# Performance work log

Measured on AMD Instinct MI355X. Metric: run time of the kernel, lower is better.

The kernel has to match this reference:

```python
import jax, jax.numpy as jnp
import numpy as np

N = 100_000   # nodes
E = 1_600_000 # edges (COO, directed as given)
D = 128       # input feature dim
H = 128       # hidden dim
L = 3         # layers


def setup_inputs() -> dict:
    key = jax.random.key(0)
    ks = jax.random.split(key, 2 + 2 * L)
    x = jax.random.normal(ks[0], (N, D), dtype=jnp.float32)
    edge_index = jax.random.randint(ks[1], (2, E), 0, N, dtype=jnp.int32)
    inp = {"x": x, "edge_index": edge_index}
    dims = [(D, H), (H, H), (H, H)]
    for i, (fi, fo) in enumerate(dims):
        scale = 1.0 / np.sqrt(fi)
        inp[f"W{i}"] = jax.random.uniform(ks[2 + 2 * i], (fi, fo), jnp.float32, -scale, scale)
        inp[f"b{i}"] = jax.random.uniform(ks[3 + 2 * i], (fo,), jnp.float32, -scale, scale)
    return inp


def reference(x, edge_index, W0, b0, W1, b1, W2, b2):
    n = x.shape[0]
    src, dst = edge_index[0], edge_index[1]
    # GCNConv default: add self-loops, symmetric D^{-1/2}(A+I)D^{-1/2} normalization
    loop = jnp.arange(n, dtype=edge_index.dtype)
    src = jnp.concatenate([src, loop])
    dst = jnp.concatenate([dst, loop])
    ones = jnp.ones(src.shape[0], dtype=x.dtype)
    deg = jax.ops.segment_sum(ones, dst, num_segments=n)          # [N]
    dinv = jnp.where(deg > 0, jax.lax.rsqrt(deg), 0.0)            # deg^{-1/2}, inf->0
    norm = dinv[src] * dinv[dst]                                  # [E+N]

    def gcn_conv(h, W, b):
        h = h @ W                                  # linear transform first (PyG order)
        msg = h[src] * norm[:, None]               # gather + scale, [E+N, H]
        return jax.ops.segment_sum(msg, dst, num_segments=n) + b

    for W, b in ((W0, b0), (W1, b1), (W2, b2)):
        x = jax.nn.relu(gcn_conv(x, W, b))
    return x
```

## Files before the change

### kernel.cpp

```cpp
#include <hip/hip_runtime.h>
#include <hip/hip_bf16.h>

#define TPB 256

typedef short s8v __attribute__((ext_vector_type(8)));
typedef float f4v __attribute__((ext_vector_type(4)));
typedef _Float16 h8v __attribute__((ext_vector_type(8)));

#define PB 128
#define BSHIFT 10
#define BSPAN 1024
#define PCHUNK 4096

__device__ __forceinline__ unsigned short bf16_rne(float v) {
    unsigned int u = __float_as_uint(v);
    u += 0x7fffu + ((u >> 16) & 1u);
    return (unsigned short)(u >> 16);
}
__device__ __forceinline__ void split_bf16(float v, unsigned short& hi, unsigned short& lo) {
    hi = bf16_rne(v);
    float hf = __uint_as_float((unsigned int)hi << 16);
    lo = bf16_rne(v - hf);
}


__global__ __launch_bounds__(256) void bhist_kernel(const int* __restrict__ dst, int E,
                                                    int* __restrict__ bsize) {
    __shared__ int h[PB];
    int t = threadIdx.x;
    if (t < PB) h[t] = 0;
    __syncthreads();
    for (int e = blockIdx.x * 256 + t; e < E; e += gridDim.x * 256)
        atomicAdd(&h[dst[e] >> BSHIFT], 1);
    __syncthreads();
    if (t < PB && h[t] > 0) atomicAdd(&bsize[t], h[t]);
}

__global__ void bscan_kernel(const int* __restrict__ bsize, int* __restrict__ bbase,
                             int* __restrict__ bcursor, int* __restrict__ row, int n, int E) {
    __shared__ int wtot[2];
    int t = threadIdx.x;
    int sz = bsize[t];
    int lane = t & 63, wid = t >> 6;
    int v = sz;
    for (int off = 1; off < 64; off <<= 1) {
        int u = __shfl_up(v, off);
        if (lane >= off) v += u;
    }
    if (lane == 63) wtot[wid] = v;
    __syncthreads();
    if (wid == 1) v += wtot[0];
    bbase[t + 1] = v;
    bcursor[t] = v - sz;
    if (t == 0) { bbase[0] = 0; row[n] = E; }
}

__global__ __launch_bounds__(256) void partition_kernel(const int* __restrict__ src,
                                                        const int* __restrict__ dst, int E,
                                                        int* __restrict__ bcursor,
                                                        int2* __restrict__ part) {
    __shared__ int h[PB];
    __shared__ int gofs[PB];
    int t = threadIdx.x;
    long base = (long)blockIdx.x * PCHUNK;
    int cnt = (int)min((long)PCHUNK, (long)E - base);

    if (t < PB) h[t] = 0;
    __syncthreads();
    for (int j = t; j < cnt; j += 256)
        atomicAdd(&h[dst[base + j] >> BSHIFT], 1);
    __syncthreads();
    if (t < PB) gofs[t] = (h[t] > 0) ? atomicAdd(&bcursor[t], h[t]) : 0;
    __syncthreads();
    if (t < PB) h[t] = 0;
    __syncthreads();
    for (int j = t; j < cnt; j += 256) {
        int s = src[base + j], d = dst[base + j];
        int b = d >> BSHIFT;
        int idx = atomicAdd(&h[b], 1);
        part[(long)gofs[b] + idx] = make_int2(s, d);
    }
}

__global__ __launch_bounds__(1024) void csr_kernel(const int2* __restrict__ part,
                                                   const int* __restrict__ bbase,
                                                   int* __restrict__ row, float* __restrict__ dinv,
                                                   int* __restrict__ esrc, int n) {
    __shared__ int deg[BSPAN];
    __shared__ int lrow[BSPAN];
    __shared__ int cur[BSPAN];
    __shared__ int wsum[16];
    int b = blockIdx.x;
    int n0 = b << BSHIFT;
    int nn = min(BSPAN, n - n0);
    if (nn <= 0) return;
    int e0 = bbase[b], e1 = bbase[b + 1];
    int t = threadIdx.x;

    deg[t] = 0;
    __syncthreads();
    for (int e = e0 + t; e < e1; e += 1024)
        atomicAdd(&deg[part[e].y - n0], 1);
    __syncthreads();

    int a = deg[t];
    int lane = t & 63, wid = t >> 6;
    int v = a;
    for (int off = 1; off < 64; off <<= 1) {
        int u = __shfl_up(v, off);
        if (lane >= off) v += u;
    }
    if (lane == 63) wsum[wid] = v;
    __syncthreads();
    if (wid == 0 && lane < 16) {
        int w = wsum[lane];
        for (int off = 1; off < 16; off <<= 1) {
            int u = __shfl_up(w, off);
            if (lane >= off) w += u;
        }
        wsum[lane] = w;
    }
    __syncthreads();
    int excl = v - a + ((wid > 0) ? wsum[wid - 1] : 0);
    lrow[t] = excl;
    cur[t] = 0;
    if (t < nn) {
        row[n0 + t] = e0 + excl;
        dinv[n0 + t] = rsqrtf((float)(deg[t] + 1));
    }
    __syncthreads();

    for (int e = e0 + t; e < e1; e += 1024) {
        int2 p = part[e];
        int d = p.y - n0;
        int idx = atomicAdd(&cur[d], 1);
        esrc[e0 + lrow[d] + idx] = p.x;
    }
}


__global__ void wsplit_kernel(const float* __restrict__ W0, const float* __restrict__ W1,
                              const float* __restrict__ W2,
                              unsigned short* __restrict__ Whi, unsigned short* __restrict__ Wlo) {
    int t = blockIdx.x * TPB + threadIdx.x;
    if (t >= 3 * 16384) return;
    int layer = t >> 14;
    int e = t & 16383;
    int k = e >> 7, ncol = e & 127;
    const float* W = (layer == 0) ? W0 : (layer == 1) ? W1 : W2;
    unsigned short hi, lo;
    split_bf16(W[e], hi, lo);
    int ct = ncol >> 4;
    int lane = (((k >> 3) & 3) << 4) | (ncol & 15);
    int kki = k >> 5;
    int j = k & 7;
    int idx = layer * 16384 + (((ct * 4 + kki) * 64 + lane) * 8 + j);
    Whi[idx] = hi; Wlo[idx] = lo;
}


template <bool F32IN>
__global__ __launch_bounds__(256, 2) void gemm_mfma(const float* __restrict__ Xf,
                                                    const unsigned short* __restrict__ Ahg,
                                                    const unsigned short* __restrict__ Alg,
                                                    const unsigned short* __restrict__ Whs,
                                                    const unsigned short* __restrict__ Wls,
                                                    _Float16* __restrict__ Ch, int n) {
    int t = threadIdx.x;
    int wave = t >> 6, lane = t & 63;
    int ch = wave & 1, rh = wave >> 1;
    int lm = lane & 15, q = lane >> 4;
    long row0 = (long)blockIdx.x * 128 + rh * 64;

    const s8v* Wh8 = (const s8v*)Whs;
    const s8v* Wl8 = (const s8v*)Wls;
    s8v Bh[4][4], Bl[4][4];
#pragma unroll
    for (int ct = 0; ct < 4; ct++)
#pragma unroll
        for (int kki = 0; kki < 4; kki++) {
            int idx = (((ch * 4 + ct) * 4 + kki) * 64) + lane;
            Bh[ct][kki] = Wh8[idx];
            Bl[ct][kki] = Wl8[idx];
        }

    f4v acc[4][4];
#pragma unroll
    for (int rt = 0; rt < 4; rt++)
#pragma unroll
        for (int ct = 0; ct < 4; ct++) acc[rt][ct] = (f4v)0.0f;

    const s8v* A8h = (const s8v*)Ahg;
    const s8v* A8l = (const s8v*)Alg;

#pragma unroll
    for (int kki = 0; kki < 4; kki++) {
        s8v ah[4], al[4];
#pragma unroll
        for (int rt = 0; rt < 4; rt++) {
            long r = row0 + rt * 16 + lm;
            if (F32IN) {
                long rr = (r < n) ? r : (n - 1);
                const float4* xf4 = (const float4*)(Xf + rr * 128 + kki * 32 + q * 8);
                float4 u0 = xf4[0], u1 = xf4[1];
                float uf[8] = {u0.x, u0.y, u0.z, u0.w, u1.x, u1.y, u1.z, u1.w};
                s8v hv, lv;
#pragma unroll
                for (int j = 0; j < 8; j++) {
                    unsigned short hh, ll;
                    split_bf16(uf[j], hh, ll);
                    hv[j] = (short)hh; lv[j] = (short)ll;
                }
                ah[rt] = hv; al[rt] = lv;
            } else {
                long base = r * 16 + kki * 4 + q;
                ah[rt] = A8h[base];
                al[rt] = A8l[base];
            }
        }
#pragma unroll
        for (int rt = 0; rt < 4; rt++)
#pragma unroll
            for (int ct = 0; ct < 4; ct++) {
                acc[rt][ct] = __builtin_amdgcn_mfma_f32_16x16x32_bf16(ah[rt], Bh[ct][kki], acc[rt][ct], 0, 0, 0);
                acc[rt][ct] = __builtin_amdgcn_mfma_f32_16x16x32_bf16(ah[rt], Bl[ct][kki], acc[rt][ct], 0, 0, 0);
                acc[rt][ct] = __builtin_amdgcn_mfma_f32_16x16x32_bf16(al[rt], Bh[ct][kki], acc[rt][ct], 0, 0, 0);
            }
    }

#pragma unroll
    for (int rt = 0; rt < 4; rt++) {
        long rbase = row0 + rt * 16 + q * 4;
#pragma unroll
        for (int reg = 0; reg < 4; reg++) {
            long r = rbase + reg;
            if (r < n) {
#pragma unroll
                for (int ct = 0; ct < 4; ct++)
                    Ch[r * 128 + ch * 64 + ct * 16 + lm] = (_Float16)acc[rt][ct][reg];
            }
        }
    }
}


template <bool SPLIT>
__global__ __launch_bounds__(256) void agg_kernel(const h8v* __restrict__ hH,
                                                  const float* __restrict__ dinv,
                                                  const int* __restrict__ row,
                                                  const int* __restrict__ esrc,
                                                  const float* __restrict__ bias,
                                                  float* __restrict__ out,
                                                  unsigned short* __restrict__ ohi,
                                                  unsigned short* __restrict__ olo, int n) {
    int g    = threadIdx.x >> 4;
    int lane = threadIdx.x & 15;
    int i = blockIdx.x * 16 + g;
    if (i >= n) return;

    float di = dinv[i];
    float s2 = di * di;

    h8v self = hH[(size_t)i * 16 + lane];
    float acc[8];
#pragma unroll
    for (int k = 0; k < 8; k++) acc[k] = (float)self[k] * s2;

    int e0 = row[i], e1 = row[i + 1];
    int e = e0;

    for (; e + 4 <= e1; e += 4) {
        int s0 = esrc[e + 0];
        int s1 = esrc[e + 1];
        int s2i = esrc[e + 2];
        int s3 = esrc[e + 3];
        h8v v0 = hH[(size_t)s0 * 16 + lane];
        h8v v1 = hH[(size_t)s1 * 16 + lane];
        h8v v2 = hH[(size_t)s2i * 16 + lane];
        h8v v3 = hH[(size_t)s3 * 16 + lane];
        float w0 = dinv[s0] * di;
        float w1 = dinv[s1] * di;
        float w2 = dinv[s2i] * di;
        float w3 = dinv[s3] * di;
#pragma unroll
        for (int k = 0; k < 8; k++)
            acc[k] += w0 * (float)v0[k] + w1 * (float)v1[k] + w2 * (float)v2[k] + w3 * (float)v3[k];
    }
    for (; e < e1; ++e) {
        int s = esrc[e];
        h8v v = hH[(size_t)s * 16 + lane];
        float w = dinv[s] * di;
#pragma unroll
        for (int k = 0; k < 8; k++) acc[k] += w * (float)v[k];
    }

    const float4* b4 = (const float4*)(bias + lane * 8);
    float4 bA = b4[0], bB = b4[1];
    float o[8];
    o[0] = fmaxf(acc[0] + bA.x, 0.f); o[1] = fmaxf(acc[1] + bA.y, 0.f);
    o[2] = fmaxf(acc[2] + bA.z, 0.f); o[3] = fmaxf(acc[3] + bA.w, 0.f);
    o[4] = fmaxf(acc[4] + bB.x, 0.f); o[5] = fmaxf(acc[5] + bB.y, 0.f);
    o[6] = fmaxf(acc[6] + bB.z, 0.f); o[7] = fmaxf(acc[7] + bB.w, 0.f);

    if (SPLIT) {
        ushort4 h0, l0, h1, l1;
        split_bf16(o[0], h0.x, l0.x); split_bf16(o[1], h0.y, l0.y);
        split_bf16(o[2], h0.z, l0.z); split_bf16(o[3], h0.w, l0.w);
        split_bf16(o[4], h1.x, l1.x); split_bf16(o[5], h1.y, l1.y);
        split_bf16(o[6], h1.z, l1.z); split_bf16(o[7], h1.w, l1.w);
        ushort4* oh = (ushort4*)(ohi + (size_t)i * 128 + lane * 8);
        ushort4* ol = (ushort4*)(olo + (size_t)i * 128 + lane * 8);
        oh[0] = h0; oh[1] = h1;
        ol[0] = l0; ol[1] = l1;
    } else {
        float4* o4 = (float4*)(out + (size_t)i * 128 + lane * 8);
        o4[0] = make_float4(o[0], o[1], o[2], o[3]);
        o4[1] = make_float4(o[4], o[5], o[6], o[7]);
    }
}


extern "C" void kernel_launch(void* const* d_in, const int* in_sizes, int n_in,
                              void* d_out, int out_size, void* d_ws, size_t ws_size,
                              hipStream_t stream) {
    const float* x  = (const float*)d_in[0];
    const int*   ei = (const int*)d_in[1];
    const float* W0 = (const float*)d_in[2];
    const float* b0 = (const float*)d_in[3];
    const float* W1 = (const float*)d_in[4];
    const float* b1 = (const float*)d_in[5];
    const float* W2 = (const float*)d_in[6];
    const float* b2 = (const float*)d_in[7];

    const int H = 128;
    int n = in_sizes[0] / H;
    int E = in_sizes[1] / 2;
    const int* srcp = ei;
    const int* dstp = ei + E;

    int gemm_blocks = (n + 127) / 128;
    long npad = (long)gemm_blocks * 128;
    int nbuck = (n + BSPAN - 1) >> BSHIFT;

    char* p = (char*)d_ws;
    auto alloc = [&](size_t bytes) {
        void* r = (void*)p;
        p += (bytes + 255) & ~(size_t)255;
        return r;
    };
    _Float16* bufH = (_Float16*)alloc((size_t)npad * H * 2);
    unsigned short* sh = (unsigned short*)alloc((size_t)npad * H * 2);
    unsigned short* sl = (unsigned short*)alloc((size_t)npad * H * 2);
    unsigned short* Whs = (unsigned short*)alloc(3 * 16384 * 2);
    unsigned short* Wls = (unsigned short*)alloc(3 * 16384 * 2);
    float* dinv  = (float*)alloc((size_t)n * sizeof(float));
    int*  row    = (int*)alloc((size_t)(n + 1) * sizeof(int));
    int*  bsize  = (int*)alloc(PB * sizeof(int));
    int*  bbase  = (int*)alloc((PB + 1) * sizeof(int));
    int*  bcursor= (int*)alloc(PB * sizeof(int));
    int2* part   = (int2*)alloc((size_t)E * sizeof(int2));
    int*  esrc   = (int*)alloc((size_t)E * sizeof(int));

    hipMemsetAsync(bsize, 0, PB * sizeof(int), stream);

    bhist_kernel<<<1024, 256, 0, stream>>>(dstp, E, bsize);
    bscan_kernel<<<1, PB, 0, stream>>>(bsize, bbase, bcursor, row, n, E);
    partition_kernel<<<(E + PCHUNK - 1) / PCHUNK, 256, 0, stream>>>(srcp, dstp, E, bcursor, part);
    csr_kernel<<<nbuck, 1024, 0, stream>>>(part, bbase, row, dinv, esrc, n);

    wsplit_kernel<<<(3 * 16384 + TPB - 1) / TPB, TPB, 0, stream>>>(W0, W1, W2, Whs, Wls);

    float* out = (float*)d_out;
    int agg_blocks = (n + 15) / 16;
    const h8v* hH = (const h8v*)bufH;

    gemm_mfma<true><<<gemm_blocks, 256, 0, stream>>>(x, nullptr, nullptr, Whs, Wls, bufH, n);
    agg_kernel<true><<<agg_blocks, 256, 0, stream>>>(hH, dinv, row, esrc, b0, nullptr, sh, sl, n);
    gemm_mfma<false><<<gemm_blocks, 256, 0, stream>>>(nullptr, sh, sl, Whs + 16384, Wls + 16384, bufH, n);
    agg_kernel<true><<<agg_blocks, 256, 0, stream>>>(hH, dinv, row, esrc, b1, nullptr, sh, sl, n);
    gemm_mfma<false><<<gemm_blocks, 256, 0, stream>>>(nullptr, sh, sl, Whs + 32768, Wls + 32768, bufH, n);
    agg_kernel<false><<<agg_blocks, 256, 0, stream>>>(hH, dinv, row, esrc, b2, out, nullptr, nullptr, n);
}
```

Baseline: 462.7 us.

## Fuse aggregation with next layer's GEMM and stage GEMM output through LDS

```diff
diff --git a/kernel.cpp b/kernel.cpp
--- a/kernel.cpp
+++ b/kernel.cpp
@@ -159,13 +159,11 @@
 }
 
 
-template <bool F32IN>
-__global__ __launch_bounds__(256, 2) void gemm_mfma(const float* __restrict__ Xf,
-                                                    const unsigned short* __restrict__ Ahg,
-                                                    const unsigned short* __restrict__ Alg,
-                                                    const unsigned short* __restrict__ Whs,
-                                                    const unsigned short* __restrict__ Wls,
-                                                    _Float16* __restrict__ Ch, int n) {
+__global__ __launch_bounds__(256, 2) void gemm0_mfma(const float* __restrict__ Xf,
+                                                     const unsigned short* __restrict__ Whs,
+                                                     const unsigned short* __restrict__ Wls,
+                                                     _Float16* __restrict__ Ch, int n) {
+    __shared__ _Float16 Oh[128 * 128];
     int t = threadIdx.x;
     int wave = t >> 6, lane = t & 63;
     int ch = wave & 1, rh = wave >> 1;
@@ -190,33 +188,24 @@
 #pragma unroll
         for (int ct = 0; ct < 4; ct++) acc[rt][ct] = (f4v)0.0f;
 
-    const s8v* A8h = (const s8v*)Ahg;
-    const s8v* A8l = (const s8v*)Alg;
-
 #pragma unroll
     for (int kki = 0; kki < 4; kki++) {
         s8v ah[4], al[4];
 #pragma unroll
         for (int rt = 0; rt < 4; rt++) {
             long r = row0 + rt * 16 + lm;
-            if (F32IN) {
-                long rr = (r < n) ? r : (n - 1);
-                const float4* xf4 = (const float4*)(Xf + rr * 128 + kki * 32 + q * 8);
-                float4 u0 = xf4[0], u1 = xf4[1];
-                float uf[8] = {u0.x, u0.y, u0.z, u0.w, u1.x, u1.y, u1.z, u1.w};
-                s8v hv, lv;
-#pragma unroll
-                for (int j = 0; j < 8; j++) {
-                    unsigned short hh, ll;
-                    split_bf16(uf[j], hh, ll);
-                    hv[j] = (short)hh; lv[j] = (short)ll;
-                }
-                ah[rt] = hv; al[rt] = lv;
-            } else {
-                long base = r * 16 + kki * 4 + q;
-                ah[rt] = A8h[base];
-                al[rt] = A8l[base];
+            long rr = (r < n) ? r : (n - 1);
+            const float4* xf4 = (const float4*)(Xf + rr * 128 + kki * 32 + q * 8);
+            float4 u0 = xf4[0], u1 = xf4[1];
+            float uf[8] = {u0.x, u0.y, u0.z, u0.w, u1.x, u1.y, u1.z, u1.w};
+            s8v hv, lv;
+#pragma unroll
+            for (int j = 0; j < 8; j++) {
+                unsigned short hh, ll;
+                split_bf16(uf[j], hh, ll);
+                hv[j] = (short)hh; lv[j] = (short)ll;
             }
+            ah[rt] = hv; al[rt] = lv;
         }
 #pragma unroll
         for (int rt = 0; rt < 4; rt++)
@@ -229,30 +218,155 @@
     }
 
 #pragma unroll
-    for (int rt = 0; rt < 4; rt++) {
-        long rbase = row0 + rt * 16 + q * 4;
+    for (int rt = 0; rt < 4; rt++)
 #pragma unroll
         for (int reg = 0; reg < 4; reg++) {
-            long r = rbase + reg;
-            if (r < n) {
-#pragma unroll
-                for (int ct = 0; ct < 4; ct++)
-                    Ch[r * 128 + ch * 64 + ct * 16 + lm] = (_Float16)acc[rt][ct][reg];
-            }
-        }
-    }
-}
-
-
-template <bool SPLIT>
-__global__ __launch_bounds__(256) void agg_kernel(const h8v* __restrict__ hH,
-                                                  const float* __restrict__ dinv,
-                                                  const int* __restrict__ row,
-                                                  const int* __restrict__ esrc,
-                                                  const float* __restrict__ bias,
-                                                  float* __restrict__ out,
-                                                  unsigned short* __restrict__ ohi,
-                                                  unsigned short* __restrict__ olo, int n) {
+            int lr = rh * 64 + rt * 16 + q * 4 + reg;
+#pragma unroll
+            for (int ct = 0; ct < 4; ct++)
+                Oh[lr * 128 + ch * 64 + ct * 16 + lm] = (_Float16)acc[rt][ct][reg];
+        }
+    __syncthreads();
+
+    long rowb = (long)blockIdx.x * 128;
+    int lr = t >> 1;
+    int cb = (t & 1) * 64;
+    if (rowb + lr < n) {
+        const uint4* s = (const uint4*)&Oh[lr * 128 + cb];
+        uint4* d = (uint4*)&Ch[(rowb + lr) * 128 + cb];
+#pragma unroll
+        for (int u = 0; u < 8; u++) d[u] = s[u];
+    }
+}
+
+
+__global__ __launch_bounds__(256) void fused_kernel(const h8v* __restrict__ hIn,
+                                                    const float* __restrict__ dinv,
+                                                    const int* __restrict__ row,
+                                                    const int* __restrict__ esrc,
+                                                    const float* __restrict__ bias,
+                                                    const unsigned short* __restrict__ Whs,
+                                                    const unsigned short* __restrict__ Wls,
+                                                    _Float16* __restrict__ hOut, int n) {
+    __shared__ float As[16 * 132];
+    int t = threadIdx.x;
+    int g = t >> 4, lane = t & 15;
+    long i = (long)blockIdx.x * 16 + g;
+
+    float r[8];
+    if (i < n) {
+        float di = dinv[i];
+        float s2 = di * di;
+        h8v self = hIn[i * 16 + lane];
+        float acc[8];
+#pragma unroll
+        for (int k = 0; k < 8; k++) acc[k] = (float)self[k] * s2;
+
+        int e0 = row[i], e1 = row[i + 1];
+        int e = e0;
+        for (; e + 4 <= e1; e += 4) {
+            int s0 = esrc[e + 0];
+            int s1 = esrc[e + 1];
+            int s2i = esrc[e + 2];
+            int s3 = esrc[e + 3];
+            h8v v0 = hIn[(size_t)s0 * 16 + lane];
+            h8v v1 = hIn[(size_t)s1 * 16 + lane];
+            h8v v2 = hIn[(size_t)s2i * 16 + lane];
+            h8v v3 = hIn[(size_t)s3 * 16 + lane];
+            float w0 = dinv[s0] * di;
+            float w1 = dinv[s1] * di;
+            float w2 = dinv[s2i] * di;
+            float w3 = dinv[s3] * di;
+#pragma unroll
+            for (int k = 0; k < 8; k++)
+                acc[k] += w0 * (float)v0[k] + w1 * (float)v1[k] + w2 * (float)v2[k] + w3 * (float)v3[k];
+        }
+        for (; e < e1; ++e) {
+            int s = esrc[e];
+            h8v v = hIn[(size_t)s * 16 + lane];
+            float w = dinv[s] * di;
+#pragma unroll
+            for (int k = 0; k < 8; k++) acc[k] += w * (float)v[k];
+        }
+
+        const float4* b4 = (const float4*)(bias + lane * 8);
+        float4 bA = b4[0], bB = b4[1];
+        r[0] = fmaxf(acc[0] + bA.x, 0.f); r[1] = fmaxf(acc[1] + bA.y, 0.f);
+        r[2] = fmaxf(acc[2] + bA.z, 0.f); r[3] = fmaxf(acc[3] + bA.w, 0.f);
+        r[4] = fmaxf(acc[4] + bB.x, 0.f); r[5] = fmaxf(acc[5] + bB.y, 0.f);
+        r[6] = fmaxf(acc[6] + bB.z, 0.f); r[7] = fmaxf(acc[7] + bB.w, 0.f);
+    } else {
+#pragma unroll
+        for (int k = 0; k < 8; k++) r[k] = 0.f;
+    }
+
+    float* dstA = &As[g * 132 + lane * 8];
+    *(float4*)dstA = make_float4(r[0], r[1], r[2], r[3]);
+    *(float4*)(dstA + 4) = make_float4(r[4], r[5], r[6], r[7]);
+    __syncthreads();
+
+    int w = t >> 6, l64 = t & 63;
+    int lm = l64 & 15, q = l64 >> 4;
+
+    const s8v* Wh8 = (const s8v*)Whs;
+    const s8v* Wl8 = (const s8v*)Wls;
+    s8v Bh[2][4], Bl[2][4];
+#pragma unroll
+    for (int c = 0; c < 2; c++)
+#pragma unroll
+        for (int kki = 0; kki < 4; kki++) {
+            int idx = (((w * 2 + c) * 4 + kki) * 64) + l64;
+            Bh[c][kki] = Wh8[idx];
+            Bl[c][kki] = Wl8[idx];
+        }
+
+    f4v acc2[2];
+    acc2[0] = (f4v)0.0f; acc2[1] = (f4v)0.0f;
+
+#pragma unroll
+    for (int kki = 0; kki < 4; kki++) {
+        const float* ap = &As[lm * 132 + kki * 32 + q * 8];
+        float4 u0 = *(const float4*)ap;
+        float4 u1 = *(const float4*)(ap + 4);
+        float uf[8] = {u0.x, u0.y, u0.z, u0.w, u1.x, u1.y, u1.z, u1.w};
+        s8v hv, lv;
+#pragma unroll
+        for (int j = 0; j < 8; j++) {
+            unsigned short hh, ll;
+            split_bf16(uf[j], hh, ll);
+            hv[j] = (short)hh; lv[j] = (short)ll;
+        }
+#pragma unroll
+        for (int c = 0; c < 2; c++) {
+            acc2[c] = __builtin_amdgcn_mfma_f32_16x16x32_bf16(hv, Bh[c][kki], acc2[c], 0, 0, 0);
+            acc2[c] = __builtin_amdgcn_mfma_f32_16x16x32_bf16(hv, Bl[c][kki], acc2[c], 0, 0, 0);
+            acc2[c] = __builtin_amdgcn_mfma_f32_16x16x32_bf16(lv, Bh[c][kki], acc2[c], 0, 0, 0);
+        }
+    }
+    __syncthreads();
+
+    _Float16* Oh = (_Float16*)As;
+#pragma unroll
+    for (int c = 0; c < 2; c++)
+#pragma unroll
+        for (int reg = 0; reg < 4; reg++)
+            Oh[(q * 4 + reg) * 128 + (w * 2 + c) * 16 + lm] = (_Float16)acc2[c][reg];
+    __syncthreads();
+
+    long gi = (long)blockIdx.x * 16 + (t >> 4);
+    if (gi < n) {
+        uint4 v = *(const uint4*)&Oh[t * 8];
+        *(uint4*)&hOut[gi * 128 + (size_t)(t & 15) * 8] = v;
+    }
+}
+
+
+__global__ __launch_bounds__(256) void agg_final(const h8v* __restrict__ hH,
+                                                 const float* __restrict__ dinv,
+                                                 const int* __restrict__ row,
+                                                 const int* __restrict__ esrc,
+                                                 const float* __restrict__ bias,
+                                                 float* __restrict__ out, int n) {
     int g    = threadIdx.x >> 4;
     int lane = threadIdx.x & 15;
     int i = blockIdx.x * 16 + g;
@@ -268,7 +382,6 @@
 
     int e0 = row[i], e1 = row[i + 1];
     int e = e0;
-
     for (; e + 4 <= e1; e += 4) {
         int s0 = esrc[e + 0];
         int s1 = esrc[e + 1];
@@ -296,27 +409,11 @@
 
     const float4* b4 = (const float4*)(bias + lane * 8);
     float4 bA = b4[0], bB = b4[1];
-    float o[8];
-    o[0] = fmaxf(acc[0] + bA.x, 0.f); o[1] = fmaxf(acc[1] + bA.y, 0.f);
-    o[2] = fmaxf(acc[2] + bA.z, 0.f); o[3] = fmaxf(acc[3] + bA.w, 0.f);
-    o[4] = fmaxf(acc[4] + bB.x, 0.f); o[5] = fmaxf(acc[5] + bB.y, 0.f);
-    o[6] = fmaxf(acc[6] + bB.z, 0.f); o[7] = fmaxf(acc[7] + bB.w, 0.f);
-
-    if (SPLIT) {
-        ushort4 h0, l0, h1, l1;
-        split_bf16(o[0], h0.x, l0.x); split_bf16(o[1], h0.y, l0.y);
-        split_bf16(o[2], h0.z, l0.z); split_bf16(o[3], h0.w, l0.w);
-        split_bf16(o[4], h1.x, l1.x); split_bf16(o[5], h1.y, l1.y);
-        split_bf16(o[6], h1.z, l1.z); split_bf16(o[7], h1.w, l1.w);
-        ushort4* oh = (ushort4*)(ohi + (size_t)i * 128 + lane * 8);
-        ushort4* ol = (ushort4*)(olo + (size_t)i * 128 + lane * 8);
-        oh[0] = h0; oh[1] = h1;
-        ol[0] = l0; ol[1] = l1;
-    } else {
-        float4* o4 = (float4*)(out + (size_t)i * 128 + lane * 8);
-        o4[0] = make_float4(o[0], o[1], o[2], o[3]);
-        o4[1] = make_float4(o[4], o[5], o[6], o[7]);
-    }
+    float4* o4 = (float4*)(out + (size_t)i * 128 + lane * 8);
+    o4[0] = make_float4(fmaxf(acc[0] + bA.x, 0.f), fmaxf(acc[1] + bA.y, 0.f),
+                        fmaxf(acc[2] + bA.z, 0.f), fmaxf(acc[3] + bA.w, 0.f));
+    o4[1] = make_float4(fmaxf(acc[4] + bB.x, 0.f), fmaxf(acc[5] + bB.y, 0.f),
+                        fmaxf(acc[6] + bB.z, 0.f), fmaxf(acc[7] + bB.w, 0.f));
 }
 
 
@@ -348,9 +445,8 @@
         p += (bytes + 255) & ~(size_t)255;
         return r;
     };
-    _Float16* bufH = (_Float16*)alloc((size_t)npad * H * 2);
-    unsigned short* sh = (unsigned short*)alloc((size_t)npad * H * 2);
-    unsigned short* sl = (unsigned short*)alloc((size_t)npad * H * 2);
+    _Float16* bufH0 = (_Float16*)alloc((size_t)npad * H * 2);
+    _Float16* bufH1 = (_Float16*)alloc((size_t)npad * H * 2);
     unsigned short* Whs = (unsigned short*)alloc(3 * 16384 * 2);
     unsigned short* Wls = (unsigned short*)alloc(3 * 16384 * 2);
     float* dinv  = (float*)alloc((size_t)n * sizeof(float));
@@ -371,13 +467,12 @@
     wsplit_kernel<<<(3 * 16384 + TPB - 1) / TPB, TPB, 0, stream>>>(W0, W1, W2, Whs, Wls);
 
     float* out = (float*)d_out;
-    int agg_blocks = (n + 15) / 16;
-    const h8v* hH = (const h8v*)bufH;
-
-    gemm_mfma<true><<<gemm_blocks, 256, 0, stream>>>(x, nullptr, nullptr, Whs, Wls, bufH, n);
-    agg_kernel<true><<<agg_blocks, 256, 0, stream>>>(hH, dinv, row, esrc, b0, nullptr, sh, sl, n);
-    gemm_mfma<false><<<gemm_blocks, 256, 0, stream>>>(nullptr, sh, sl, Whs + 16384, Wls + 16384, bufH, n);
-    agg_kernel<true><<<agg_blocks, 256, 0, stream>>>(hH, dinv, row, esrc, b1, nullptr, sh, sl, n);
-    gemm_mfma<false><<<gemm_blocks, 256, 0, stream>>>(nullptr, sh, sl, Whs + 32768, Wls + 32768, bufH, n);
-    agg_kernel<false><<<agg_blocks, 256, 0, stream>>>(hH, dinv, row, esrc, b2, out, nullptr, nullptr, n);
-}
+    int node_blocks = (n + 15) / 16;
+
+    gemm0_mfma<<<gemm_blocks, 256, 0, stream>>>(x, Whs, Wls, bufH0, n);
+    fused_kernel<<<node_blocks, 256, 0, stream>>>((const h8v*)bufH0, dinv, row, esrc, b0,
+                                                  Whs + 16384, Wls + 16384, bufH1, n);
+    fused_kernel<<<node_blocks, 256, 0, stream>>>((const h8v*)bufH1, dinv, row, esrc, b1,
+                                                  Whs + 32768, Wls + 32768, bufH0, n);
+    agg_final<<<node_blocks, 256, 0, stream>>>((const h8v*)bufH0, dinv, row, esrc, b2, out, n);
+}
```

Result: faster. 409.5 us (-11.5%).
